# Performance work log

Measured on AMD Instinct MI355X. Metric: run time of the kernel, lower is better.

## Reference

```python
import jax, jax.numpy as jnp
import numpy as np

B, C, H, W = 4, 512, 64, 64
MID = C // 8  # 64


def setup_inputs() -> dict:
    key = jax.random.key(0)
    ks = jax.random.split(key, 8)
    s = 0.02
    return {
        "x": jax.random.normal(ks[0], (B, C, H, W), dtype=jnp.float32),
        "Wq": jax.random.normal(ks[1], (MID, C), dtype=jnp.float32) * s,
        "bq": jax.random.normal(ks[2], (MID,), dtype=jnp.float32) * s,
        "Wk": jax.random.normal(ks[3], (MID, C), dtype=jnp.float32) * s,
        "bk": jax.random.normal(ks[4], (MID,), dtype=jnp.float32) * s,
        "Wv": jax.random.normal(ks[5], (C, C), dtype=jnp.float32) * s,
        "bv": jax.random.normal(ks[6], (C,), dtype=jnp.float32) * s,
        "gamma": jax.random.uniform(ks[7], (1,), dtype=jnp.float32),
    }


def reference(x, Wq, bq, Wk, bk, Wv, bv, gamma):
    b, c, h, w = x.shape
    n = h * w
    xf = x.reshape(b, c, n)  # [B, C, N]
    # 1x1 convs are per-position linear maps
    q = jnp.einsum('mc,bcn->bnm', Wq, xf) + bq            # [B, N, mid]
    k = jnp.einsum('mc,bcn->bmn', Wk, xf) + bk[:, None]   # [B, mid, N]
    sim = jax.nn.softmax(jnp.einsum('bnm,bmj->bnj', q, k), axis=-1)  # [B, N, N]
    v = jnp.einsum('dc,bcn->bdn', Wv, xf) + bv[:, None]   # [B, C, N]
    # feat[:, d, i] = sum_j v[:, d, j] * sim[:, i, j]
    feat = jnp.einsum('bdj,bij->bdi', v, sim)             # [B, C, N]
    out = gamma[0] * feat + xf
    return out.reshape(b, c, h, w)
```

## Files before the change

### kernel.cpp

```cpp
#include <hip/hip_runtime.h>

#define BATCH 4
#define CCH   512
#define NN    4096
#define MIDD  64

typedef unsigned short u16;
typedef unsigned int   u32;
typedef short s8v  __attribute__((ext_vector_type(8)));
typedef float f16v __attribute__((ext_vector_type(16)));

__device__ __forceinline__ u16 f2bf(float f) {
  u32 u = __float_as_uint(f);
  u += 0x7fffu + ((u >> 16) & 1u);
  return (u16)(u >> 16);
}

__device__ __forceinline__ void g2lds16(const u16* g, u16* l) {
  __builtin_amdgcn_global_load_lds(
      (const __attribute__((address_space(1))) u32*)(const void*)g,
      (__attribute__((address_space(3))) u32*)(void*)l, 16, 0, 0);
}

#define S_WAITCNT(vm, lgkm) \
  __builtin_amdgcn_s_waitcnt(((vm) & 15) | (((vm) >> 4) << 14) | (0x7 << 4) | ((lgkm) << 8))

__global__ __launch_bounds__(256) void prep_w(
    const float* __restrict__ Wq, const float* __restrict__ Wk,
    const float* __restrict__ Wv, u16* __restrict__ Wb)
{
  int e = (blockIdx.x * 256 + threadIdx.x) * 8;
  const float* src;
  if (e < 64 * 512)       src = Wq + e;
  else if (e < 128 * 512) src = Wk + (e - 64 * 512);
  else                    src = Wv + (e - 128 * 512);
  float4 v0 = *(const float4*)src;
  float4 v1 = *(const float4*)(src + 4);
  uint4 p;
  p.x = (u32)f2bf(v0.x) | ((u32)f2bf(v0.y) << 16);
  p.y = (u32)f2bf(v0.z) | ((u32)f2bf(v0.w) << 16);
  p.z = (u32)f2bf(v1.x) | ((u32)f2bf(v1.y) << 16);
  p.w = (u32)f2bf(v1.z) | ((u32)f2bf(v1.w) << 16);
  *(uint4*)(Wb + e) = p;
}

__global__ __launch_bounds__(256) void transpose_cast(
    const float* __restrict__ x, u16* __restrict__ xbT)
{
  const int b  = blockIdx.z;
  const int c0 = blockIdx.y * 64;
  const int n0 = blockIdx.x * 64;
  const int t  = threadIdx.x;
  __shared__ float ts[64 * 65];

  #pragma unroll
  for (int k = 0; k < 4; k++) {
    int idx = t + 256 * k;
    int cc = idx >> 4, n4 = idx & 15;
    float4 v = *(const float4*)&x[((size_t)(b * CCH + c0 + cc)) * NN + n0 + n4 * 4];
    float* p = &ts[cc * 65 + n4 * 4];
    p[0] = v.x; p[1] = v.y; p[2] = v.z; p[3] = v.w;
  }
  __syncthreads();

  const int n = t >> 2, cb = (t & 3) * 16;
  u16 tmp[16];
  #pragma unroll
  for (int j = 0; j < 16; j++) tmp[j] = f2bf(ts[(cb + j) * 65 + n]);
  u16* dst = &xbT[((size_t)b * NN + n0 + n) * CCH + c0 + cb];
  *(uint4*)&dst[0] = *(uint4*)&tmp[0];
  *(uint4*)&dst[8] = *(uint4*)&tmp[8];
}

__global__ __launch_bounds__(256, 2) void proj_gemm(
    const u16* __restrict__ xbT, const u16* __restrict__ Wb,
    const float* __restrict__ bq, const float* __restrict__ bk,
    const float* __restrict__ bv,
    u16* __restrict__ qT, u16* __restrict__ kT, u16* __restrict__ vT)
{
  const int b  = blockIdx.z;
  const int mt = blockIdx.y;
  const int n0 = blockIdx.x * 256;
  const int t  = threadIdx.x;
  const int ln = t & 31, hi = (t & 63) >> 5, w = t >> 6;
  const int l  = t & 63;
  const int l2 = l & 3, lr = l >> 2;
  const int swc = (l2 ^ (lr & 3)) * 8;

  const int mrow0 = (mt < 8) ? (128 + mt * 64) : ((mt == 8) ? 0 : 64);
  const float* bias = (mt < 8) ? (bv + mt * 64) : ((mt == 8) ? bq : bk);

  __shared__ u16 ws[2][64 * 32];
  __shared__ u16 xs[2][256 * 32];

  const u16* xsrc = xbT + ((size_t)b * NN + n0 + w * 64 + lr) * CCH + swc;
  const u16* wsrc = Wb + (size_t)(mrow0 + w * 16 + lr) * 512 + swc;

  f16v acc[4];
  #pragma unroll
  for (int i = 0; i < 4; i++)
    #pragma unroll
    for (int r = 0; r < 16; r++) acc[i][r] = 0.f;

  #pragma unroll
  for (int i = 0; i < 4; i++)
    g2lds16(xsrc + (size_t)(16 * i) * CCH, &xs[0][(w * 64 + i * 16) * 32]);
  g2lds16(wsrc, &ws[0][w * 16 * 32]);

  for (int it = 0; it < 16; it++) {
    const int cur = it & 1, nxt = cur ^ 1;
    __builtin_amdgcn_s_barrier();
    const int c1 = ((it + 1) & 15) * 32;
    #pragma unroll
    for (int i = 0; i < 4; i++)
      g2lds16(xsrc + (size_t)(16 * i) * CCH + c1, &xs[nxt][(w * 64 + i * 16) * 32]);
    g2lds16(wsrc + c1, &ws[nxt][w * 16 * 32]);

    S_WAITCNT(5, 15);
    __builtin_amdgcn_s_barrier();

    #pragma unroll
    for (int ks = 0; ks < 2; ks++) {
      const int cb = ((2 * ks + hi) ^ (ln & 3)) << 3;
      s8v a0 = *(const s8v*)&ws[cur][(ln)           * 32 + cb];
      s8v a1 = *(const s8v*)&ws[cur][(32 + ln)      * 32 + cb];
      s8v b0 = *(const s8v*)&xs[cur][(w * 64 + ln)      * 32 + cb];
      s8v b1 = *(const s8v*)&xs[cur][(w * 64 + 32 + ln) * 32 + cb];
      acc[0] = __builtin_amdgcn_mfma_f32_32x32x16_bf16(a0, b0, acc[0], 0, 0, 0);
      acc[1] = __builtin_amdgcn_mfma_f32_32x32x16_bf16(a0, b1, acc[1], 0, 0, 0);
      acc[2] = __builtin_amdgcn_mfma_f32_32x32x16_bf16(a1, b0, acc[2], 0, 0, 0);
      acc[3] = __builtin_amdgcn_mfma_f32_32x32x16_bf16(a1, b1, acc[3], 0, 0, 0);
    }
  }

  S_WAITCNT(0, 0);
  __builtin_amdgcn_s_barrier();

  if (mt < 8) {
    const int m0g = mt * 64;
    #pragma unroll
    for (int mi = 0; mi < 2; mi++)
      #pragma unroll
      for (int ni = 0; ni < 2; ni++) {
        f16v& a = acc[mi * 2 + ni];
        #pragma unroll
        for (int r = 0; r < 16; r++) {
          int row = (r & 3) + 8 * (r >> 2) + 4 * hi;
          int m   = mi * 32 + row;
          float val = a[r] + bias[m];
          vT[((size_t)b * CCH + m0g + m) * NN + n0 + w * 64 + ni * 32 + ln] = f2bf(val);
        }
      }
  } else {
    u16* dst = (mt == 8) ? qT : kT;
    u16* xt  = &xs[0][0];
    #pragma unroll
    for (int mi = 0; mi < 2; mi++)
      #pragma unroll
      for (int ni = 0; ni < 2; ni++) {
        f16v& a = acc[mi * 2 + ni];
        #pragma unroll
        for (int r = 0; r < 16; r++) {
          int row = (r & 3) + 8 * (r >> 2) + 4 * hi;
          int m   = mi * 32 + row;
          int nr  = w * 64 + ni * 32 + ln;
          xt[(nr << 6) + (((m >> 3) ^ (ln & 7)) << 3) + (m & 7)] = f2bf(a[r] + bias[m]);
        }
      }
    __syncthreads();
    const int r7 = t & 7;
    u16* drow = &dst[((size_t)b * NN + n0 + t) * 64];
    #pragma unroll
    for (int k = 0; k < 8; k++)
      *(uint4*)&drow[k * 8] = *(uint4*)&xt[(t << 6) + ((k ^ r7) << 3)];
  }
}

__global__ __launch_bounds__(256, 2) void attn_kernel(
    const u16* __restrict__ qT,
    const u16* __restrict__ kT,
    const u16* __restrict__ vT,
    const float* __restrict__ x,
    const float* __restrict__ gamma,
    float* __restrict__ out)
{
  __shared__ u16 ksm[2][64 * 64];
  __shared__ u16 plm[2][64 * 64];

  const int bx    = blockIdx.x;
  const int slot  = bx & 7;
  const int b     = slot >> 1;
  const int dbase = (slot & 1) * 256;
  const int i0    = (bx >> 3) * 64;
  const int t     = threadIdx.x;
  const int l     = t & 63, ln = l & 31, hi = l >> 5;
  const int w     = t >> 6;
  const int qh    = w >> 1;
  const int jh    = w & 1;
  const int l3    = l & 7, lh3 = l >> 3;
  const int sw8   = (l3 ^ lh3) * 8;

  s8v qfrag[4];
  {
    const u16* qp = qT + ((size_t)b * NN + i0 + qh * 32 + ln) * 64 + hi * 8;
    #pragma unroll
    for (int k = 0; k < 4; k++) qfrag[k] = *(const s8v*)(qp + 16 * k);
  }

  const u16* kbase = kT + (size_t)b * NN * 64;
  const u16* ksrc  = kbase + (size_t)(16 * w + lh3) * 64 + sw8;
  const u16* vrow0 = vT + ((size_t)b * CCH + dbase + w * 32 + ln) * NN + hi * 8;
  const u16* vrow1 = vrow0 + (size_t)128 * NN;

  f16v oacc[4];
  #pragma unroll
  for (int i = 0; i < 4; i++)
    #pragma unroll
    for (int r = 0; r < 16; r++) oacc[i][r] = 0.f;
  float lpart[16];
  #pragma unroll
  for (int r = 0; r < 16; r++) lpart[r] = 0.f;

  #pragma unroll
  for (int i = 0; i < 2; i++)
    g2lds16(ksrc + (size_t)(8 * i) * 64, &ksm[0][(w * 2 + i) * 512]);

  for (int it = 0; it < 64; it++) {
    const int j0  = it * 64;
    const int cur = it & 1, nxt = cur ^ 1;

    s8v vf0[4], vf1[4];
    {
      const u16* vp0 = vrow0 + j0;
      const u16* vp1 = vrow1 + j0;
      #pragma unroll
      for (int ks = 0; ks < 4; ks++) {
        vf0[ks] = *(const s8v*)(vp0 + 16 * ks);
        vf1[ks] = *(const s8v*)(vp1 + 16 * ks);
      }
    }

    const int j1 = ((it + 1) & 63) * 64;
    #pragma unroll
    for (int i = 0; i < 2; i++)
      g2lds16(ksrc + (size_t)(j1 + 8 * i) * 64, &ksm[nxt][(w * 2 + i) * 512]);

    S_WAITCNT(10, 15);
    __builtin_amdgcn_s_barrier();

    f16v sacc;
    #pragma unroll
    for (int r = 0; r < 16; r++) sacc[r] = 0.f;
    #pragma unroll
    for (int ks = 0; ks < 4; ks++) {
      s8v bf = *(const s8v*)&ksm[cur][(jh * 32 + ln) * 64 + (((2 * ks + hi) ^ l3) << 3)];
      sacc = __builtin_amdgcn_mfma_f32_32x32x16_bf16(qfrag[ks], bf, sacc, 0, 0, 0);
    }
    #pragma unroll
    for (int r = 0; r < 16; r++) {
      float p = __expf(sacc[r]);
      lpart[r] += p;
      int row = qh * 32 + (r & 3) + ((r >> 2) << 3) + (hi << 2);
      int r7  = (r & 3) + (hi << 2);
      int jbl = (jh << 2) + (ln >> 3);
      plm[cur][(row << 6) + ((jbl ^ r7) << 3) + (ln & 7)] = f2bf(p);
    }

    S_WAITCNT(2, 0);
    __builtin_amdgcn_s_barrier();

    #pragma unroll
    for (int ks = 0; ks < 4; ks++) {
      const int cb = ((2 * ks + hi) ^ l3) << 3;
      s8v p0 = *(const s8v*)&plm[cur][(ln << 6) + cb];
      s8v p1 = *(const s8v*)&plm[cur][((32 + ln) << 6) + cb];
      oacc[0] = __builtin_amdgcn_mfma_f32_32x32x16_bf16(vf0[ks], p0, oacc[0], 0, 0, 0);
      oacc[1] = __builtin_amdgcn_mfma_f32_32x32x16_bf16(vf0[ks], p1, oacc[1], 0, 0, 0);
      oacc[2] = __builtin_amdgcn_mfma_f32_32x32x16_bf16(vf1[ks], p0, oacc[2], 0, 0, 0);
      oacc[3] = __builtin_amdgcn_mfma_f32_32x32x16_bf16(vf1[ks], p1, oacc[3], 0, 0, 0);
    }
  }

  S_WAITCNT(0, 0);
  __builtin_amdgcn_s_barrier();

  float* lred = (float*)&ksm[0][0];
  #pragma unroll
  for (int r = 0; r < 16; r++) {
    float v = lpart[r];
    v += __shfl_xor(v, 1);  v += __shfl_xor(v, 2);  v += __shfl_xor(v, 4);
    v += __shfl_xor(v, 8);  v += __shfl_xor(v, 16);
    lpart[r] = v;
  }
  if (ln == 0) {
    #pragma unroll
    for (int r = 0; r < 16; r++) {
      int row = qh * 32 + (r & 3) + ((r >> 2) << 3) + (hi << 2);
      lred[jh * 64 + row] = lpart[r];
    }
  }
  __syncthreads();

  const float g0 = gamma[0];
  #pragma unroll
  for (int qt = 0; qt < 2; qt++) {
    const float linv = 1.0f / (lred[qt * 32 + ln] + lred[64 + qt * 32 + ln]);
    const int n = i0 + qt * 32 + ln;
    #pragma unroll
    for (int ds = 0; ds < 2; ds++) {
      f16v& a = oacc[ds * 2 + qt];
      const int dg = dbase + (w + 4 * ds) * 32;
      #pragma unroll
      for (int r = 0; r < 16; r++) {
        int dl = (r & 3) + 8 * (r >> 2) + 4 * hi;
        size_t idx = ((size_t)b * CCH + dg + dl) * NN + n;
        out[idx] = g0 * a[r] * linv + x[idx];
      }
    }
  }
}

extern "C" void kernel_launch(void* const* d_in, const int* in_sizes, int n_in,
                              void* d_out, int out_size, void* d_ws, size_t ws_size,
                              hipStream_t stream) {
  const float* x     = (const float*)d_in[0];
  const float* Wq    = (const float*)d_in[1];
  const float* bq    = (const float*)d_in[2];
  const float* Wk    = (const float*)d_in[3];
  const float* bk    = (const float*)d_in[4];
  const float* Wv    = (const float*)d_in[5];
  const float* bv    = (const float*)d_in[6];
  const float* gamma = (const float*)d_in[7];
  float* out = (float*)d_out;

  u16* qT  = (u16*)d_ws;
  u16* kT  = qT  + (size_t)BATCH * NN * MIDD;
  u16* vT  = kT  + (size_t)BATCH * NN * MIDD;
  u16* xbT = vT  + (size_t)BATCH * CCH * NN;
  u16* Wb  = xbT + (size_t)BATCH * NN * CCH;

  prep_w<<<dim3(160), 256, 0, stream>>>(Wq, Wk, Wv, Wb);
  transpose_cast<<<dim3(NN / 64, CCH / 64, BATCH), 256, 0, stream>>>(x, xbT);
  proj_gemm<<<dim3(NN / 256, 10, BATCH), 256, 0, stream>>>(
      xbT, Wb, bq, bk, bv, qT, kT, vT);
  attn_kernel<<<dim3(512), 256, 0, stream>>>(qT, kT, vT, x, gamma, out);
}
```

Measured before the change: 257.3 us.

## Store V in MFMA fragment-packed layout so attention loads are contiguous

The projection kernel now stages each V tile through shared memory with an XOR swizzle and writes it in a fragment-major layout that matches the per-lane operand order of the MFMA in the attention kernel. The attention kernel then reads each lane's 16-byte V fragments from consecutive addresses, instead of strided rows that span the whole sequence. This is meant to coalesce V global reads in the hot loop and to make the projection's V stores vector-wide. It adds an LDS round trip and a barrier to the projection epilogue.

New measurement: 223.9 us. 13.0% less time.

```diff
diff --git a/kernel.cpp b/kernel.cpp
--- a/kernel.cpp
+++ b/kernel.cpp
@@ -76,7 +76,7 @@
     const u16* __restrict__ xbT, const u16* __restrict__ Wb,
     const float* __restrict__ bq, const float* __restrict__ bk,
     const float* __restrict__ bv,
-    u16* __restrict__ qT, u16* __restrict__ kT, u16* __restrict__ vT)
+    u16* __restrict__ qT, u16* __restrict__ kT, u16* __restrict__ vF)
 {
   const int b  = blockIdx.z;
   const int mt = blockIdx.y;
@@ -137,7 +137,7 @@
   __builtin_amdgcn_s_barrier();
 
   if (mt < 8) {
-    const int m0g = mt * 64;
+    u16* xt = &xs[0][0];
     #pragma unroll
     for (int mi = 0; mi < 2; mi++)
       #pragma unroll
@@ -147,9 +147,22 @@
         for (int r = 0; r < 16; r++) {
           int row = (r & 3) + 8 * (r >> 2) + 4 * hi;
           int m   = mi * 32 + row;
-          float val = a[r] + bias[m];
-          vT[((size_t)b * CCH + m0g + m) * NN + n0 + w * 64 + ni * 32 + ln] = f2bf(val);
+          int nr  = w * 64 + ni * 32 + ln;
+          int c8  = nr >> 3;
+          xt[m * 256 + ((c8 ^ (m & 31)) << 3) + (nr & 7)] = f2bf(a[r] + bias[m]);
         }
+      }
+    __syncthreads();
+    const int jt0 = n0 >> 6;
+    const size_t dgb = ((size_t)b * 64 + jt0 + w) * 16 + mt * 2;
+    #pragma unroll
+    for (int mh = 0; mh < 2; mh++)
+      #pragma unroll
+      for (int ks = 0; ks < 4; ks++) {
+        int c8 = w * 8 + ks * 2 + hi;
+        int m  = mh * 32 + ln;
+        s8v vv = *(const s8v*)&xt[m * 256 + ((c8 ^ ln) << 3)];
+        *(s8v*)&vF[(((dgb + mh) * 4 + ks) * 64 + l) * 8] = vv;
       }
   } else {
     u16* dst = (mt == 8) ? qT : kT;
@@ -179,7 +192,7 @@
 __global__ __launch_bounds__(256, 2) void attn_kernel(
     const u16* __restrict__ qT,
     const u16* __restrict__ kT,
-    const u16* __restrict__ vT,
+    const u16* __restrict__ vF,
     const float* __restrict__ x,
     const float* __restrict__ gamma,
     float* __restrict__ out)
@@ -209,8 +222,8 @@
 
   const u16* kbase = kT + (size_t)b * NN * 64;
   const u16* ksrc  = kbase + (size_t)(16 * w + lh3) * 64 + sw8;
-  const u16* vrow0 = vT + ((size_t)b * CCH + dbase + w * 32 + ln) * NN + hi * 8;
-  const u16* vrow1 = vrow0 + (size_t)128 * NN;
+  const u16* vfb = vF + (size_t)b * (64 * 16 * 4 * 64 * 8);
+  const int dg0  = (slot & 1) * 8 + w;
 
   f16v oacc[4];
   #pragma unroll
@@ -226,17 +239,15 @@
     g2lds16(ksrc + (size_t)(8 * i) * 64, &ksm[0][(w * 2 + i) * 512]);
 
   for (int it = 0; it < 64; it++) {
-    const int j0  = it * 64;
     const int cur = it & 1, nxt = cur ^ 1;
 
     s8v vf0[4], vf1[4];
     {
-      const u16* vp0 = vrow0 + j0;
-      const u16* vp1 = vrow1 + j0;
+      const u16* vp0 = vfb + (size_t)(it * 16 + dg0) * (4 * 64 * 8) + l * 8;
       #pragma unroll
       for (int ks = 0; ks < 4; ks++) {
-        vf0[ks] = *(const s8v*)(vp0 + 16 * ks);
-        vf1[ks] = *(const s8v*)(vp1 + 16 * ks);
+        vf0[ks] = *(const s8v*)(vp0 + ks * (64 * 8));
+        vf1[ks] = *(const s8v*)(vp0 + 4 * (4 * 64 * 8) + ks * (64 * 8));
       }
     }
 
@@ -335,13 +346,13 @@
 
   u16* qT  = (u16*)d_ws;
   u16* kT  = qT  + (size_t)BATCH * NN * MIDD;
-  u16* vT  = kT  + (size_t)BATCH * NN * MIDD;
-  u16* xbT = vT  + (size_t)BATCH * CCH * NN;
+  u16* vF  = kT  + (size_t)BATCH * NN * MIDD;
+  u16* xbT = vF  + (size_t)BATCH * CCH * NN;
   u16* Wb  = xbT + (size_t)BATCH * NN * CCH;
 
   prep_w<<<dim3(160), 256, 0, stream>>>(Wq, Wk, Wv, Wb);
   transpose_cast<<<dim3(NN / 64, CCH / 64, BATCH), 256, 0, stream>>>(x, xbT);
   proj_gemm<<<dim3(NN / 256, 10, BATCH), 256, 0, stream>>>(
-      xbT, Wb, bq, bk, bv, qT, kT, vT);
-  attn_kernel<<<dim3(512), 256, 0, stream>>>(qT, kT, vT, x, gamma, out);
-}
+      xbT, Wb, bq, bk, bv, qT, kT, vF);
+  attn_kernel<<<dim3(512), 256, 0, stream>>>(qT, kT, vF, x, gamma, out);
+}
```
